# Performance work log

Measured on AMD Instinct MI355X. Metric: run time of the kernel, lower is better.

Reference implementation:

```python
import jax, jax.numpy as jnp
import numpy as np

LAYERS, BLOCKS = 10, 4
NL = LAYERS * BLOCKS
RC, DC, SC, OUT_C = 32, 32, 256, 256
B, T = 4, 32768


def setup_inputs() -> dict:
    key = jax.random.key(0)
    ks = jax.random.split(key, 6)
    s = 0.1  # keep tanh out of saturation
    return {
        "x": jax.random.normal(ks[0], (B, 1, T), jnp.float32),
        "W_start": jax.random.normal(ks[1], (RC, 1), jnp.float32) * s,
        "b_start": jnp.zeros((RC,), jnp.float32),
        "Wd": jax.random.normal(ks[2], (NL, DC, RC, 2), jnp.float32) * s,  # torch conv1d weight (out,in,k)
        "bd": jnp.zeros((NL, DC), jnp.float32),
        "Wr": jax.random.normal(ks[3], (NL, RC, DC), jnp.float32) * s,     # 1x1 residual convs
        "br": jnp.zeros((NL, RC), jnp.float32),
        "Ws": jax.random.normal(ks[4], (NL, SC, DC), jnp.float32) * s,     # 1x1 skip convs
        "bs": jnp.zeros((NL, SC), jnp.float32),
        "Wf": jax.random.normal(ks[5], (OUT_C, SC), jnp.float32) * s,      # final 1x1 conv
        "bf": jnp.zeros((OUT_C,), jnp.float32),
    }


def _forward(x, W_start, b_start, Wd, bd, Wr, br, Ws, bs, Wf, bf):
    # start 1x1 conv: [B,1,T] -> [B,RC,T]
    h = jnp.einsum('oi,bit->bot', W_start, x) + b_start[:, None]
    skip = jnp.zeros((x.shape[0], SC, x.shape[2]), x.dtype)
    for i in range(NL):  # fixed small layer loop (40)
        d = 2 ** (i % LAYERS)
        # causal dilated conv, kernel=2: out[t] = W[...,0]@x[t-d] + W[...,1]@x[t]
        h_shift = jnp.pad(h, ((0, 0), (0, 0), (d, 0)))[:, :, : h.shape[2]]
        z = (jnp.einsum('oi,bit->bot', Wd[i, :, :, 1], h)
             + jnp.einsum('oi,bit->bot', Wd[i, :, :, 0], h_shift)
             + bd[i][:, None])
        z = jnp.tanh(z)
        r = jnp.einsum('oi,bit->bot', Wr[i], z) + br[i][:, None]
        h = h + r  # residual connection
        skip = skip + jnp.einsum('oi,bit->bot', Ws[i], h) + bs[i][:, None]
    out = jax.nn.relu(skip)
    return jnp.einsum('oi,bit->bot', Wf, out) + bf[:, None]


def reference(x, W_start, b_start, Wd, bd, Wr, br, Ws, bs, Wf, bf):
    return _forward(x, W_start, b_start, Wd, bd, Wr, br, Ws, bs, Wf, bf)
```

## Files before the change

### kernel.cpp

```cpp
#include <hip/hip_runtime.h>
#include <hip/hip_bf16.h>

#define T_LEN 32768
#define B_N   4
#define RC    32
#define DC    32
#define SC    256
#define OUTC  256
#define NL    40
#define KTOT  (NL * RC)
#define NBT   (B_N * T_LEN)
#define SLOTB ((size_t)NBT * 32 * 2)
#define BTW   128
#define RING  24576

typedef float f32x4 __attribute__((ext_vector_type(4)));
typedef short bf16x8 __attribute__((ext_vector_type(8)));
typedef __attribute__((address_space(3))) unsigned int lds_u32;
typedef __attribute__((address_space(3))) char lds_char;
typedef __attribute__((address_space(1))) unsigned int glb_u32;

__device__ __forceinline__ unsigned short f2bf_bits(float f) {
    __hip_bfloat16 b = __float2bfloat16(f);
    unsigned short u;
    __builtin_memcpy(&u, &b, 2);
    return u;
}
__device__ __forceinline__ unsigned pack2(float a, float b) {
    return (unsigned)f2bf_bits(a) | ((unsigned)f2bf_bits(b) << 16);
}
__device__ __forceinline__ float bflo(unsigned u) { return __uint_as_float((u & 0xFFFFu) << 16); }
__device__ __forceinline__ float bfhi(unsigned u) { return __uint_as_float(u & 0xFFFF0000u); }
__device__ __forceinline__ float ftanh(float x) {
    float e = __expf(2.f * x);
    return 1.f - 2.f / (e + 1.f);
}
__device__ __forceinline__ int swz(int L) { return L ^ ((((L >> 7) & 3)) << 4); }

__global__ __launch_bounds__(256) void k_prep(const float* __restrict__ Ws,
                                              const float* __restrict__ Wf,
                                              const float* __restrict__ Wd,
                                              const float* __restrict__ Wr,
                                              const float* __restrict__ bs,
                                              unsigned short* __restrict__ Wsk2,
                                              unsigned short* __restrict__ Wfk,
                                              unsigned short* __restrict__ Wd1k,
                                              unsigned short* __restrict__ Wd0k,
                                              unsigned short* __restrict__ Wrk,
                                              float* __restrict__ bs_sum) {
    int g = blockIdx.x * 256 + threadIdx.x;
    if (g < SC * KTOT) {
        int i = g >> 13, r = g & 8191;
        int oc = r >> 5, c = r & 31;
        Wsk2[g] = f2bf_bits(Ws[(i * SC + oc) * RC + c]);
        return;
    }
    g -= SC * KTOT;
    if (g < OUTC * SC) { Wfk[g] = f2bf_bits(Wf[g]); return; }
    g -= OUTC * SC;
    if (g < NL * 1024) {
        int i = g >> 10, r = g & 1023;
        int o = r >> 5, c = r & 31;
        Wd1k[g] = f2bf_bits(Wd[((i * DC + o) * RC + c) * 2 + 1]);
        return;
    }
    g -= NL * 1024;
    if (g < NL * 1024) {
        int i = g >> 10, r = g & 1023;
        int o = r >> 5, c = r & 31;
        Wd0k[g] = f2bf_bits(Wd[((i * DC + o) * RC + c) * 2 + 0]);
        return;
    }
    g -= NL * 1024;
    if (g < NL * 1024) { Wrk[g] = f2bf_bits(Wr[g]); return; }
    g -= NL * 1024;
    if (g < SC) {
        float s = 0.f;
        for (int i = 0; i < NL; ++i) s += bs[i * SC + g];
        bs_sum[g] = s;
    }
}

__global__ __launch_bounds__(256) void k_start(const float* __restrict__ x,
                                               const float* __restrict__ Wst,
                                               const float* __restrict__ bst,
                                               unsigned short* __restrict__ h0) {
    int g = blockIdx.x * 256 + threadIdx.x;
    float xv = x[g];
    unsigned u[16];
#pragma unroll
    for (int q = 0; q < 16; ++q) {
        float a = Wst[2 * q] * xv + bst[2 * q];
        float b = Wst[2 * q + 1] * xv + bst[2 * q + 1];
        u[q] = pack2(a, b);
    }
    unsigned short* op = h0 + (size_t)g * 32;
#pragma unroll
    for (int q = 0; q < 4; ++q) *(uint4*)&op[q * 8] = *(uint4*)&u[q * 4];
}

__global__ __launch_bounds__(256, 4) void k_layer(const unsigned short* __restrict__ hprev,
                                                  unsigned short* __restrict__ hnext,
                                                  const unsigned short* __restrict__ Wd1k,
                                                  const unsigned short* __restrict__ Wd0k,
                                                  const unsigned short* __restrict__ Wrk,
                                                  const float* __restrict__ bd,
                                                  const float* __restrict__ br,
                                                  int d) {
    __shared__ unsigned short zbuf[4][32 * 40];
    int lane = threadIdx.x & 63;
    int wq = threadIdx.x >> 6;
    int lr = lane & 15, lg = lane >> 4;
    int btb = blockIdx.x * 128 + wq * 32;
    unsigned short* zp = &zbuf[wq][0];

    bf16x8 wd1[2], wd0[2], wr[2];
#pragma unroll
    for (int m = 0; m < 2; ++m) {
        int ao = (m * 16 + lr) * 32 + 8 * lg;
        wd1[m] = *(const bf16x8*)(Wd1k + ao);
        wd0[m] = *(const bf16x8*)(Wd0k + ao);
        wr[m]  = *(const bf16x8*)(Wrk + ao);
    }

    bf16x8 hc[2], hs[2];
    uint2 hcc[2][2];
#pragma unroll
    for (int n = 0; n < 2; ++n) {
        int bt = btb + n * 16 + lr;
        int t = bt & (T_LEN - 1);
        const unsigned short* hp = hprev + (size_t)bt * 32;
        hc[n] = *(const bf16x8*)(hp + 8 * lg);
        int bts = (t >= d) ? (bt - d) : bt;
        bf16x8 v = *(const bf16x8*)(hprev + (size_t)bts * 32 + 8 * lg);
        if (t < d) v = (bf16x8){0, 0, 0, 0, 0, 0, 0, 0};
        hs[n] = v;
#pragma unroll
        for (int m = 0; m < 2; ++m) hcc[n][m] = *(const uint2*)(hp + m * 16 + 4 * lg);
    }

    f32x4 zac[2][2];
#pragma unroll
    for (int m = 0; m < 2; ++m)
#pragma unroll
        for (int n = 0; n < 2; ++n) {
            f32x4 a = __builtin_amdgcn_mfma_f32_16x16x32_bf16(wd0[m], hs[n], (f32x4){0.f, 0.f, 0.f, 0.f}, 0, 0, 0);
            zac[m][n] = __builtin_amdgcn_mfma_f32_16x16x32_bf16(wd1[m], hc[n], a, 0, 0, 0);
        }

#pragma unroll
    for (int m = 0; m < 2; ++m) {
        float4 bdv = *(const float4*)(bd + m * 16 + 4 * lg);
#pragma unroll
        for (int n = 0; n < 2; ++n) {
            int rbt = n * 16 + lr;
            float z0 = ftanh(zac[m][n][0] + bdv.x);
            float z1 = ftanh(zac[m][n][1] + bdv.y);
            float z2 = ftanh(zac[m][n][2] + bdv.z);
            float z3 = ftanh(zac[m][n][3] + bdv.w);
            uint2 u;
            u.x = pack2(z0, z1);
            u.y = pack2(z2, z3);
            *(uint2*)(zp + rbt * 40 + m * 16 + 4 * lg) = u;
        }
    }

    f32x4 racc[2][2];
#pragma unroll
    for (int n = 0; n < 2; ++n) {
        int rbt = n * 16 + lr;
        bf16x8 zb = *(const bf16x8*)(zp + rbt * 40 + 8 * lg);
#pragma unroll
        for (int m = 0; m < 2; ++m)
            racc[m][n] = __builtin_amdgcn_mfma_f32_16x16x32_bf16(wr[m], zb, (f32x4){0.f, 0.f, 0.f, 0.f}, 0, 0, 0);
    }

#pragma unroll
    for (int m = 0; m < 2; ++m) {
        float4 brv = *(const float4*)(br + m * 16 + 4 * lg);
#pragma unroll
        for (int n = 0; n < 2; ++n) {
            int bt = btb + n * 16 + lr;
            float h0 = bflo(hcc[n][m].x) + racc[m][n][0] + brv.x;
            float h1 = bfhi(hcc[n][m].x) + racc[m][n][1] + brv.y;
            float h2 = bflo(hcc[n][m].y) + racc[m][n][2] + brv.z;
            float h3 = bfhi(hcc[n][m].y) + racc[m][n][3] + brv.w;
            uint2 u;
            u.x = pack2(h0, h1);
            u.y = pack2(h2, h3);
            *(uint2*)(hnext + (size_t)bt * 32 + m * 16 + 4 * lg) = u;
        }
    }
}

__global__ __launch_bounds__(512, 4) void k_skipfinal(const unsigned short* __restrict__ hist,
                                                      const unsigned short* __restrict__ Wsk2,
                                                      const unsigned short* __restrict__ Wfk,
                                                      const float* __restrict__ bs_sum,
                                                      const float* __restrict__ bfv,
                                                      float* __restrict__ outp) {
    __shared__ char smem[65536];
    const int tid = threadIdx.x;
    const int lane = tid & 63, wq = tid >> 6;
    const int lr = lane & 15, lg = lane >> 4;
    const int wm = wq & 3, wn = wq >> 2;
    const int bt0 = blockIdx.x * BTW;
    const char* histb = (const char*)hist;
    const char* Wsb = (const char*)Wsk2;
    lds_char* smem3 = (lds_char*)smem;

    int asrc[2], bsrc;
#pragma unroll
    for (int p = 0; p < 2; ++p) asrc[p] = swz(p * 8192 + tid * 16);
    bsrc = (size_t)0;
    {
        int D = tid * 16;
        bsrc = bt0 * 64 + swz(D);
    }

    auto stage = [&](int k) {
        char* base = smem + (k & 1) * RING;
#pragma unroll
        for (int p = 0; p < 2; ++p)
            __builtin_amdgcn_global_load_lds((const glb_u32*)(Wsb + (size_t)k * 16384 + asrc[p]),
                                             (lds_u32*)(base + p * 8192 + tid * 16), 16, 0, 0);
        __builtin_amdgcn_global_load_lds((const glb_u32*)(histb + (size_t)k * SLOTB + bsrc),
                                         (lds_u32*)(base + 16384 + tid * 16), 16, 0, 0);
    };

    f32x4 acc[4][4];
#pragma unroll
    for (int m = 0; m < 4; ++m)
#pragma unroll
        for (int n = 0; n < 4; ++n) acc[m][n] = (f32x4){0.f, 0.f, 0.f, 0.f};

    const int cswz = (lg * 16) ^ (((lr >> 1) & 3) << 4);
    const int arow = wm * 64 + lr;
    const int brow = wn * 64 + lr;

    stage(0);
    stage(1);

#pragma unroll
    for (int i = 0; i < NL; ++i) {
        if (i >= 1 && i + 1 < NL) stage(i + 1);
        if (i + 1 < NL) asm volatile("s_waitcnt vmcnt(3)" ::: "memory");
        else            asm volatile("s_waitcnt vmcnt(0)" ::: "memory");
        __builtin_amdgcn_s_barrier();

        lds_char* Ab = smem3 + (i & 1) * RING;
        lds_char* Bb = Ab + 16384;
        bf16x8 af0, af1, af2, af3, bb0, bb1, bb2, bb3;
        asm volatile("ds_read_b128 %0, %1" : "=v"(af0) : "v"(Ab + (arow + 0) * 64 + cswz));
        asm volatile("ds_read_b128 %0, %1" : "=v"(af1) : "v"(Ab + (arow + 16) * 64 + cswz));
        asm volatile("ds_read_b128 %0, %1" : "=v"(af2) : "v"(Ab + (arow + 32) * 64 + cswz));
        asm volatile("ds_read_b128 %0, %1" : "=v"(af3) : "v"(Ab + (arow + 48) * 64 + cswz));
        asm volatile("ds_read_b128 %0, %1" : "=v"(bb0) : "v"(Bb + (brow + 0) * 64 + cswz));
        asm volatile("ds_read_b128 %0, %1" : "=v"(bb1) : "v"(Bb + (brow + 16) * 64 + cswz));
        asm volatile("ds_read_b128 %0, %1" : "=v"(bb2) : "v"(Bb + (brow + 32) * 64 + cswz));
        asm volatile("ds_read_b128 %0, %1" : "=v"(bb3) : "v"(Bb + (brow + 48) * 64 + cswz));
        asm volatile("s_waitcnt lgkmcnt(0)" ::: "memory");
        __builtin_amdgcn_sched_barrier(0);

        acc[0][0] = __builtin_amdgcn_mfma_f32_16x16x32_bf16(af0, bb0, acc[0][0], 0, 0, 0);
        acc[1][0] = __builtin_amdgcn_mfma_f32_16x16x32_bf16(af1, bb0, acc[1][0], 0, 0, 0);
        acc[2][0] = __builtin_amdgcn_mfma_f32_16x16x32_bf16(af2, bb0, acc[2][0], 0, 0, 0);
        acc[3][0] = __builtin_amdgcn_mfma_f32_16x16x32_bf16(af3, bb0, acc[3][0], 0, 0, 0);
        acc[0][1] = __builtin_amdgcn_mfma_f32_16x16x32_bf16(af0, bb1, acc[0][1], 0, 0, 0);
        acc[1][1] = __builtin_amdgcn_mfma_f32_16x16x32_bf16(af1, bb1, acc[1][1], 0, 0, 0);
        acc[2][1] = __builtin_amdgcn_mfma_f32_16x16x32_bf16(af2, bb1, acc[2][1], 0, 0, 0);
        acc[3][1] = __builtin_amdgcn_mfma_f32_16x16x32_bf16(af3, bb1, acc[3][1], 0, 0, 0);
        acc[0][2] = __builtin_amdgcn_mfma_f32_16x16x32_bf16(af0, bb2, acc[0][2], 0, 0, 0);
        acc[1][2] = __builtin_amdgcn_mfma_f32_16x16x32_bf16(af1, bb2, acc[1][2], 0, 0, 0);
        acc[2][2] = __builtin_amdgcn_mfma_f32_16x16x32_bf16(af2, bb2, acc[2][2], 0, 0, 0);
        acc[3][2] = __builtin_amdgcn_mfma_f32_16x16x32_bf16(af3, bb2, acc[3][2], 0, 0, 0);
        acc[0][3] = __builtin_amdgcn_mfma_f32_16x16x32_bf16(af0, bb3, acc[0][3], 0, 0, 0);
        acc[1][3] = __builtin_amdgcn_mfma_f32_16x16x32_bf16(af1, bb3, acc[1][3], 0, 0, 0);
        acc[2][3] = __builtin_amdgcn_mfma_f32_16x16x32_bf16(af2, bb3, acc[2][3], 0, 0, 0);
        acc[3][3] = __builtin_amdgcn_mfma_f32_16x16x32_bf16(af3, bb3, acc[3][3], 0, 0, 0);
        __builtin_amdgcn_s_barrier();
    }
    __syncthreads();

    char* skb = smem;
#pragma unroll
    for (int m = 0; m < 4; ++m) {
        int oc0 = wm * 64 + m * 16 + lg * 4;
        float c0 = bs_sum[oc0], c1 = bs_sum[oc0 + 1], c2 = bs_sum[oc0 + 2], c3 = bs_sum[oc0 + 3];
#pragma unroll
        for (int n = 0; n < 4; ++n) {
            int bt = wn * 64 + n * 16 + lr;
            f32x4 v = acc[m][n];
            uint2 u;
            u.x = pack2(fmaxf(v[0] + c0, 0.f), fmaxf(v[1] + c1, 0.f));
            u.y = pack2(fmaxf(v[2] + c2, 0.f), fmaxf(v[3] + c3, 0.f));
            int L = bt * 512 + oc0 * 2;
            *(uint2*)(skb + (L ^ ((bt & 7) << 4))) = u;
        }
    }
    __syncthreads();

    f32x4 acc2[4][4];
#pragma unroll
    for (int m = 0; m < 4; ++m)
#pragma unroll
        for (int n = 0; n < 4; ++n) acc2[m][n] = (f32x4){0.f, 0.f, 0.f, 0.f};

    const unsigned short* Fb = Wfk + (size_t)(wm * 64 + lr) * SC + 8 * lg;

#pragma unroll
    for (int kk = 0; kk < SC / 32; ++kk) {
        bf16x8 fa[4];
#pragma unroll
        for (int m = 0; m < 4; ++m) fa[m] = *(const bf16x8*)(Fb + (size_t)m * 16 * SC + kk * 32);
        bf16x8 sbv[4];
#pragma unroll
        for (int n = 0; n < 4; ++n) {
            int bt = wn * 64 + n * 16 + lr;
            int L = bt * 512 + kk * 64 + lg * 16;
            sbv[n] = *(const bf16x8*)(skb + (L ^ ((bt & 7) << 4)));
        }
#pragma unroll
        for (int m = 0; m < 4; ++m)
#pragma unroll
            for (int n = 0; n < 4; ++n)
                acc2[m][n] = __builtin_amdgcn_mfma_f32_16x16x32_bf16(fa[m], sbv[n], acc2[m][n], 0, 0, 0);
    }

    int b2 = bt0 >> 15;
    int t0 = bt0 & (T_LEN - 1);
#pragma unroll
    for (int m = 0; m < 4; ++m) {
        int o0 = wm * 64 + m * 16 + lg * 4;
        float q0 = bfv[o0], q1 = bfv[o0 + 1], q2 = bfv[o0 + 2], q3 = bfv[o0 + 3];
#pragma unroll
        for (int n = 0; n < 4; ++n) {
            int t = t0 + wn * 64 + n * 16 + lr;
            f32x4 v = acc2[m][n];
            outp[((size_t)(b2 * OUTC + o0 + 0) << 15) + t] = v[0] + q0;
            outp[((size_t)(b2 * OUTC + o0 + 1) << 15) + t] = v[1] + q1;
            outp[((size_t)(b2 * OUTC + o0 + 2) << 15) + t] = v[2] + q2;
            outp[((size_t)(b2 * OUTC + o0 + 3) << 15) + t] = v[3] + q3;
        }
    }
}

extern "C" void kernel_launch(void* const* d_in, const int* in_sizes, int n_in,
                              void* d_out, int out_size, void* d_ws, size_t ws_size,
                              hipStream_t stream) {
    const float* x       = (const float*)d_in[0];
    const float* W_start = (const float*)d_in[1];
    const float* b_start = (const float*)d_in[2];
    const float* Wd      = (const float*)d_in[3];
    const float* bd      = (const float*)d_in[4];
    const float* Wr      = (const float*)d_in[5];
    const float* br      = (const float*)d_in[6];
    const float* Ws      = (const float*)d_in[7];
    const float* bs      = (const float*)d_in[8];
    const float* Wf      = (const float*)d_in[9];
    const float* bfv     = (const float*)d_in[10];

    char* wsb = (char*)d_ws;
    unsigned short* Wsk2 = (unsigned short*)(wsb);
    unsigned short* Wfk  = (unsigned short*)(wsb + 655360);
    unsigned short* Wd1k = (unsigned short*)(wsb + 786432);
    unsigned short* Wd0k = (unsigned short*)(wsb + 868352);
    unsigned short* Wrk  = (unsigned short*)(wsb + 950272);
    float*          bs_sum = (float*)(wsb + 1032192);
    char* S1 = wsb + (1 << 20);
    char* X  = S1 + 40 * SLOTB;

    auto slotptr = [&](int i) -> unsigned short* {
        return (unsigned short*)(i == 0 ? X : S1 + (size_t)(i - 1) * SLOTB);
    };

    k_prep<<<(SC * KTOT + OUTC * SC + 3 * NL * 1024 + SC + 255) / 256, 256, 0, stream>>>(
        Ws, Wf, Wd, Wr, bs, Wsk2, Wfk, Wd1k, Wd0k, Wrk, bs_sum);
    k_start<<<NBT / 256, 256, 0, stream>>>(x, W_start, b_start, slotptr(0));

    for (int i = 0; i < NL; ++i) {
        int d = 1 << (i % 10);
        k_layer<<<NBT / 128, 256, 0, stream>>>(slotptr(i), slotptr(i + 1),
                                               Wd1k + i * 1024, Wd0k + i * 1024, Wrk + i * 1024,
                                               bd + i * DC, br + i * RC, d);
    }

    k_skipfinal<<<NBT / BTW, 512, 0, stream>>>((unsigned short*)S1, Wsk2, Wfk, bs_sum, bfv, (float*)d_out);
}
```

Before: 448.4 us.

## Deepen skip-GEMM prefetch pipeline and double per-wave tile in layer kernel

The skip/final kernel now keeps separate LDS rings for weight tiles (2 stages) and history tiles (4 stages). It issues the loads for later stages after the LDS reads of the current stage, so global loads overlap the MFMA work, with vmcnt waits tuned per iteration. The layer kernel processes 64 timesteps per wave instead of 32, which halves the grid and amortizes weight loads, at the cost of more registers (launch bounds lowered to 3 blocks per SIMD). The hand-counted vmcnt schedule is fragile and could race if the load counts are wrong.

```diff
diff --git a/kernel.cpp b/kernel.cpp
--- a/kernel.cpp
+++ b/kernel.cpp
@@ -12,7 +12,6 @@
 #define NBT   (B_N * T_LEN)
 #define SLOTB ((size_t)NBT * 32 * 2)
 #define BTW   128
-#define RING  24576
 
 typedef float f32x4 __attribute__((ext_vector_type(4)));
 typedef short bf16x8 __attribute__((ext_vector_type(8)));
@@ -36,6 +35,16 @@
     return 1.f - 2.f / (e + 1.f);
 }
 __device__ __forceinline__ int swz(int L) { return L ^ ((((L >> 7) & 3)) << 4); }
+__device__ __forceinline__ void wait_vmcnt(int n) {
+    switch (n) {
+        case 0: asm volatile("s_waitcnt vmcnt(0)" ::: "memory"); break;
+        case 2: asm volatile("s_waitcnt vmcnt(2)" ::: "memory"); break;
+        case 3: asm volatile("s_waitcnt vmcnt(3)" ::: "memory"); break;
+        case 4: asm volatile("s_waitcnt vmcnt(4)" ::: "memory"); break;
+        case 5: asm volatile("s_waitcnt vmcnt(5)" ::: "memory"); break;
+        default: asm volatile("s_waitcnt vmcnt(8)" ::: "memory"); break;
+    }
+}
 
 __global__ __launch_bounds__(256) void k_prep(const float* __restrict__ Ws,
                                               const float* __restrict__ Wf,
@@ -99,7 +108,7 @@
     for (int q = 0; q < 4; ++q) *(uint4*)&op[q * 8] = *(uint4*)&u[q * 4];
 }
 
-__global__ __launch_bounds__(256, 4) void k_layer(const unsigned short* __restrict__ hprev,
+__global__ __launch_bounds__(256, 3) void k_layer(const unsigned short* __restrict__ hprev,
                                                   unsigned short* __restrict__ hnext,
                                                   const unsigned short* __restrict__ Wd1k,
                                                   const unsigned short* __restrict__ Wd0k,
@@ -107,11 +116,11 @@
                                                   const float* __restrict__ bd,
                                                   const float* __restrict__ br,
                                                   int d) {
-    __shared__ unsigned short zbuf[4][32 * 40];
+    __shared__ unsigned short zbuf[4][64 * 40];
     int lane = threadIdx.x & 63;
     int wq = threadIdx.x >> 6;
     int lr = lane & 15, lg = lane >> 4;
-    int btb = blockIdx.x * 128 + wq * 32;
+    int btb = blockIdx.x * 256 + wq * 64;
     unsigned short* zp = &zbuf[wq][0];
 
     bf16x8 wd1[2], wd0[2], wr[2];
@@ -123,10 +132,10 @@
         wr[m]  = *(const bf16x8*)(Wrk + ao);
     }
 
-    bf16x8 hc[2], hs[2];
-    uint2 hcc[2][2];
-#pragma unroll
-    for (int n = 0; n < 2; ++n) {
+    bf16x8 hc[4], hs[4];
+    uint2 hcc[4][2];
+#pragma unroll
+    for (int n = 0; n < 4; ++n) {
         int bt = btb + n * 16 + lr;
         int t = bt & (T_LEN - 1);
         const unsigned short* hp = hprev + (size_t)bt * 32;
@@ -139,11 +148,11 @@
         for (int m = 0; m < 2; ++m) hcc[n][m] = *(const uint2*)(hp + m * 16 + 4 * lg);
     }
 
-    f32x4 zac[2][2];
+    f32x4 zac[2][4];
 #pragma unroll
     for (int m = 0; m < 2; ++m)
 #pragma unroll
-        for (int n = 0; n < 2; ++n) {
+        for (int n = 0; n < 4; ++n) {
             f32x4 a = __builtin_amdgcn_mfma_f32_16x16x32_bf16(wd0[m], hs[n], (f32x4){0.f, 0.f, 0.f, 0.f}, 0, 0, 0);
             zac[m][n] = __builtin_amdgcn_mfma_f32_16x16x32_bf16(wd1[m], hc[n], a, 0, 0, 0);
         }
@@ -152,7 +161,7 @@
     for (int m = 0; m < 2; ++m) {
         float4 bdv = *(const float4*)(bd + m * 16 + 4 * lg);
 #pragma unroll
-        for (int n = 0; n < 2; ++n) {
+        for (int n = 0; n < 4; ++n) {
             int rbt = n * 16 + lr;
             float z0 = ftanh(zac[m][n][0] + bdv.x);
             float z1 = ftanh(zac[m][n][1] + bdv.y);
@@ -165,9 +174,9 @@
         }
     }
 
-    f32x4 racc[2][2];
-#pragma unroll
-    for (int n = 0; n < 2; ++n) {
+    f32x4 racc[2][4];
+#pragma unroll
+    for (int n = 0; n < 4; ++n) {
         int rbt = n * 16 + lr;
         bf16x8 zb = *(const bf16x8*)(zp + rbt * 40 + 8 * lg);
 #pragma unroll
@@ -179,7 +188,7 @@
     for (int m = 0; m < 2; ++m) {
         float4 brv = *(const float4*)(br + m * 16 + 4 * lg);
 #pragma unroll
-        for (int n = 0; n < 2; ++n) {
+        for (int n = 0; n < 4; ++n) {
             int bt = btb + n * 16 + lr;
             float h0 = bflo(hcc[n][m].x) + racc[m][n][0] + brv.x;
             float h1 = bfhi(hcc[n][m].x) + racc[m][n][1] + brv.y;
@@ -209,23 +218,22 @@
     const char* Wsb = (const char*)Wsk2;
     lds_char* smem3 = (lds_char*)smem;
 
-    int asrc[2], bsrc;
+    int asrc[2];
 #pragma unroll
     for (int p = 0; p < 2; ++p) asrc[p] = swz(p * 8192 + tid * 16);
-    bsrc = (size_t)0;
-    {
-        int D = tid * 16;
-        bsrc = bt0 * 64 + swz(D);
-    }
-
-    auto stage = [&](int k) {
-        char* base = smem + (k & 1) * RING;
+    const int bsrc = bt0 * 64 + swz(tid * 16);
+
+    auto stageA = [&](int k) {
+        char* base = smem + (k & 1) * 16384;
 #pragma unroll
         for (int p = 0; p < 2; ++p)
             __builtin_amdgcn_global_load_lds((const glb_u32*)(Wsb + (size_t)k * 16384 + asrc[p]),
                                              (lds_u32*)(base + p * 8192 + tid * 16), 16, 0, 0);
+    };
+    auto stageB = [&](int k) {
+        char* base = smem + 32768 + (k & 3) * 8192;
         __builtin_amdgcn_global_load_lds((const glb_u32*)(histb + (size_t)k * SLOTB + bsrc),
-                                         (lds_u32*)(base + 16384 + tid * 16), 16, 0, 0);
+                                         (lds_u32*)(base + tid * 16), 16, 0, 0);
     };
 
     f32x4 acc[4][4];
@@ -238,18 +246,15 @@
     const int arow = wm * 64 + lr;
     const int brow = wn * 64 + lr;
 
-    stage(0);
-    stage(1);
+    stageA(0); stageA(1);
+    stageB(0); stageB(1); stageB(2); stageB(3);
+    wait_vmcnt(3);
+    __builtin_amdgcn_s_barrier();
 
 #pragma unroll
     for (int i = 0; i < NL; ++i) {
-        if (i >= 1 && i + 1 < NL) stage(i + 1);
-        if (i + 1 < NL) asm volatile("s_waitcnt vmcnt(3)" ::: "memory");
-        else            asm volatile("s_waitcnt vmcnt(0)" ::: "memory");
-        __builtin_amdgcn_s_barrier();
-
-        lds_char* Ab = smem3 + (i & 1) * RING;
-        lds_char* Bb = Ab + 16384;
+        lds_char* Ab = smem3 + (i & 1) * 16384;
+        lds_char* Bb = smem3 + 32768 + (i & 3) * 8192;
         bf16x8 af0, af1, af2, af3, bb0, bb1, bb2, bb3;
         asm volatile("ds_read_b128 %0, %1" : "=v"(af0) : "v"(Ab + (arow + 0) * 64 + cswz));
         asm volatile("ds_read_b128 %0, %1" : "=v"(af1) : "v"(Ab + (arow + 16) * 64 + cswz));
@@ -261,6 +266,10 @@
         asm volatile("ds_read_b128 %0, %1" : "=v"(bb3) : "v"(Bb + (brow + 48) * 64 + cswz));
         asm volatile("s_waitcnt lgkmcnt(0)" ::: "memory");
         __builtin_amdgcn_sched_barrier(0);
+        __builtin_amdgcn_s_barrier();
+
+        if (i + 2 < NL) stageA(i + 2);
+        if (i + 4 < NL) stageB(i + 4);
 
         acc[0][0] = __builtin_amdgcn_mfma_f32_16x16x32_bf16(af0, bb0, acc[0][0], 0, 0, 0);
         acc[1][0] = __builtin_amdgcn_mfma_f32_16x16x32_bf16(af1, bb0, acc[1][0], 0, 0, 0);
@@ -278,7 +287,12 @@
         acc[1][3] = __builtin_amdgcn_mfma_f32_16x16x32_bf16(af1, bb3, acc[1][3], 0, 0, 0);
         acc[2][3] = __builtin_amdgcn_mfma_f32_16x16x32_bf16(af2, bb3, acc[2][3], 0, 0, 0);
         acc[3][3] = __builtin_amdgcn_mfma_f32_16x16x32_bf16(af3, bb3, acc[3][3], 0, 0, 0);
-        __builtin_amdgcn_s_barrier();
+
+        if (i < NL - 1) {
+            int Nw = (i == 0) ? 5 : (i <= 35) ? 4 : (i == 36) ? 3 : (i == 37) ? 2 : 0;
+            wait_vmcnt(Nw);
+            __builtin_amdgcn_s_barrier();
+        }
     }
     __syncthreads();
 
@@ -380,7 +394,7 @@
 
     for (int i = 0; i < NL; ++i) {
         int d = 1 << (i % 10);
-        k_layer<<<NBT / 128, 256, 0, stream>>>(slotptr(i), slotptr(i + 1),
+        k_layer<<<NBT / 256, 256, 0, stream>>>(slotptr(i), slotptr(i + 1),
                                                Wd1k + i * 1024, Wd0k + i * 1024, Wrk + i * 1024,
                                                bd + i * DC, br + i * RC, d);
     }
```

Result: slower. 503.0 us (+12.2%).

## Fuse all forty residual layers into one persistent kernel with neighbor flags

Applied to the files above, without the earlier changes.

The forty per-layer launches are replaced by a single persistent kernel with one 512-thread block per (512-timestep chunk, batch). Each block runs every layer on its chunk in order. A release/acquire flag chain makes a block wait until the previous chunk has finished the prior layer, which is enough because the dilation never exceeds the chunk length. This is meant to remove per-layer launch and tail overhead and to keep each chunk's activations hot in cache between layers. In exchange the grid is much smaller, blocks are serialized along a dependency chain that adds pipeline skew, and the kernel relies on all blocks being co-resident to avoid deadlock.

```diff
diff --git a/kernel.cpp b/kernel.cpp
--- a/kernel.cpp
+++ b/kernel.cpp
@@ -99,97 +99,112 @@
     for (int q = 0; q < 4; ++q) *(uint4*)&op[q * 8] = *(uint4*)&u[q * 4];
 }
 
-__global__ __launch_bounds__(256, 4) void k_layer(const unsigned short* __restrict__ hprev,
-                                                  unsigned short* __restrict__ hnext,
-                                                  const unsigned short* __restrict__ Wd1k,
-                                                  const unsigned short* __restrict__ Wd0k,
-                                                  const unsigned short* __restrict__ Wrk,
-                                                  const float* __restrict__ bd,
-                                                  const float* __restrict__ br,
-                                                  int d) {
-    __shared__ unsigned short zbuf[4][32 * 40];
-    int lane = threadIdx.x & 63;
-    int wq = threadIdx.x >> 6;
-    int lr = lane & 15, lg = lane >> 4;
-    int btb = blockIdx.x * 128 + wq * 32;
-    unsigned short* zp = &zbuf[wq][0];
-
+__global__ __launch_bounds__(512) void k_zeroflags(int* __restrict__ flags) {
+    flags[blockIdx.x * 512 + threadIdx.x] = 0;
+}
+
+__device__ __forceinline__ void layer_step(const unsigned short* __restrict__ slotin,
+                                           unsigned short* __restrict__ slotout,
+                                           const unsigned short* __restrict__ w1p,
+                                           const unsigned short* __restrict__ w0p,
+                                           const unsigned short* __restrict__ wrp,
+                                           const float* __restrict__ bdp,
+                                           const float* __restrict__ brp,
+                                           unsigned short* zp, int tbase, int b,
+                                           int lr, int lg, int d) {
     bf16x8 wd1[2], wd0[2], wr[2];
+    float4 bdv[2], brv[2];
 #pragma unroll
     for (int m = 0; m < 2; ++m) {
         int ao = (m * 16 + lr) * 32 + 8 * lg;
-        wd1[m] = *(const bf16x8*)(Wd1k + ao);
-        wd0[m] = *(const bf16x8*)(Wd0k + ao);
-        wr[m]  = *(const bf16x8*)(Wrk + ao);
-    }
-
-    bf16x8 hc[2], hs[2];
-    uint2 hcc[2][2];
-#pragma unroll
-    for (int n = 0; n < 2; ++n) {
-        int bt = btb + n * 16 + lr;
-        int t = bt & (T_LEN - 1);
-        const unsigned short* hp = hprev + (size_t)bt * 32;
-        hc[n] = *(const bf16x8*)(hp + 8 * lg);
-        int bts = (t >= d) ? (bt - d) : bt;
-        bf16x8 v = *(const bf16x8*)(hprev + (size_t)bts * 32 + 8 * lg);
-        if (t < d) v = (bf16x8){0, 0, 0, 0, 0, 0, 0, 0};
-        hs[n] = v;
-#pragma unroll
-        for (int m = 0; m < 2; ++m) hcc[n][m] = *(const uint2*)(hp + m * 16 + 4 * lg);
-    }
-
-    f32x4 zac[2][2];
-#pragma unroll
-    for (int m = 0; m < 2; ++m)
-#pragma unroll
-        for (int n = 0; n < 2; ++n) {
-            f32x4 a = __builtin_amdgcn_mfma_f32_16x16x32_bf16(wd0[m], hs[n], (f32x4){0.f, 0.f, 0.f, 0.f}, 0, 0, 0);
-            zac[m][n] = __builtin_amdgcn_mfma_f32_16x16x32_bf16(wd1[m], hc[n], a, 0, 0, 0);
-        }
-
-#pragma unroll
-    for (int m = 0; m < 2; ++m) {
-        float4 bdv = *(const float4*)(bd + m * 16 + 4 * lg);
-#pragma unroll
-        for (int n = 0; n < 2; ++n) {
-            int rbt = n * 16 + lr;
-            float z0 = ftanh(zac[m][n][0] + bdv.x);
-            float z1 = ftanh(zac[m][n][1] + bdv.y);
-            float z2 = ftanh(zac[m][n][2] + bdv.z);
-            float z3 = ftanh(zac[m][n][3] + bdv.w);
-            uint2 u;
-            u.x = pack2(z0, z1);
-            u.y = pack2(z2, z3);
-            *(uint2*)(zp + rbt * 40 + m * 16 + 4 * lg) = u;
-        }
-    }
-
-    f32x4 racc[2][2];
-#pragma unroll
-    for (int n = 0; n < 2; ++n) {
-        int rbt = n * 16 + lr;
-        bf16x8 zb = *(const bf16x8*)(zp + rbt * 40 + 8 * lg);
-#pragma unroll
-        for (int m = 0; m < 2; ++m)
-            racc[m][n] = __builtin_amdgcn_mfma_f32_16x16x32_bf16(wr[m], zb, (f32x4){0.f, 0.f, 0.f, 0.f}, 0, 0, 0);
-    }
-
-#pragma unroll
-    for (int m = 0; m < 2; ++m) {
-        float4 brv = *(const float4*)(br + m * 16 + 4 * lg);
-#pragma unroll
-        for (int n = 0; n < 2; ++n) {
-            int bt = btb + n * 16 + lr;
-            float h0 = bflo(hcc[n][m].x) + racc[m][n][0] + brv.x;
-            float h1 = bfhi(hcc[n][m].x) + racc[m][n][1] + brv.y;
-            float h2 = bflo(hcc[n][m].y) + racc[m][n][2] + brv.z;
-            float h3 = bfhi(hcc[n][m].y) + racc[m][n][3] + brv.w;
-            uint2 u;
-            u.x = pack2(h0, h1);
-            u.y = pack2(h2, h3);
-            *(uint2*)(hnext + (size_t)bt * 32 + m * 16 + 4 * lg) = u;
-        }
+        wd1[m] = *(const bf16x8*)(w1p + ao);
+        wd0[m] = *(const bf16x8*)(w0p + ao);
+        wr[m]  = *(const bf16x8*)(wrp + ao);
+        bdv[m] = *(const float4*)(bdp + m * 16 + 4 * lg);
+        brv[m] = *(const float4*)(brp + m * 16 + 4 * lg);
+    }
+#pragma unroll
+    for (int n = 0; n < 4; ++n) {
+        int t = tbase + n * 16 + lr;
+        size_t bt = ((size_t)b << 15) + t;
+        const unsigned short* hp = slotin + bt * 32;
+        bf16x8 hc = *(const bf16x8*)(hp + 8 * lg);
+        uint2 hcc0 = *(const uint2*)(hp + 4 * lg);
+        uint2 hcc1 = *(const uint2*)(hp + 16 + 4 * lg);
+        bf16x8 hs = (bf16x8){0, 0, 0, 0, 0, 0, 0, 0};
+        if (t >= d) hs = *(const bf16x8*)(hp - (size_t)d * 32 + 8 * lg);
+
+        f32x4 z0 = __builtin_amdgcn_mfma_f32_16x16x32_bf16(wd0[0], hs, (f32x4){0.f, 0.f, 0.f, 0.f}, 0, 0, 0);
+        z0 = __builtin_amdgcn_mfma_f32_16x16x32_bf16(wd1[0], hc, z0, 0, 0, 0);
+        f32x4 z1 = __builtin_amdgcn_mfma_f32_16x16x32_bf16(wd0[1], hs, (f32x4){0.f, 0.f, 0.f, 0.f}, 0, 0, 0);
+        z1 = __builtin_amdgcn_mfma_f32_16x16x32_bf16(wd1[1], hc, z1, 0, 0, 0);
+
+        uint2 u0, u1;
+        u0.x = pack2(ftanh(z0[0] + bdv[0].x), ftanh(z0[1] + bdv[0].y));
+        u0.y = pack2(ftanh(z0[2] + bdv[0].z), ftanh(z0[3] + bdv[0].w));
+        u1.x = pack2(ftanh(z1[0] + bdv[1].x), ftanh(z1[1] + bdv[1].y));
+        u1.y = pack2(ftanh(z1[2] + bdv[1].z), ftanh(z1[3] + bdv[1].w));
+        *(uint2*)(zp + lr * 40 + 4 * lg) = u0;
+        *(uint2*)(zp + lr * 40 + 16 + 4 * lg) = u1;
+
+        bf16x8 zb = *(const bf16x8*)(zp + lr * 40 + 8 * lg);
+        f32x4 r0 = __builtin_amdgcn_mfma_f32_16x16x32_bf16(wr[0], zb, (f32x4){0.f, 0.f, 0.f, 0.f}, 0, 0, 0);
+        f32x4 r1 = __builtin_amdgcn_mfma_f32_16x16x32_bf16(wr[1], zb, (f32x4){0.f, 0.f, 0.f, 0.f}, 0, 0, 0);
+
+        uint2 o0, o1;
+        o0.x = pack2(bflo(hcc0.x) + r0[0] + brv[0].x, bfhi(hcc0.x) + r0[1] + brv[0].y);
+        o0.y = pack2(bflo(hcc0.y) + r0[2] + brv[0].z, bfhi(hcc0.y) + r0[3] + brv[0].w);
+        o1.x = pack2(bflo(hcc1.x) + r1[0] + brv[1].x, bfhi(hcc1.x) + r1[1] + brv[1].y);
+        o1.y = pack2(bflo(hcc1.y) + r1[2] + brv[1].z, bfhi(hcc1.y) + r1[3] + brv[1].w);
+        unsigned short* op = slotout + bt * 32;
+        *(uint2*)(op + 4 * lg) = o0;
+        *(uint2*)(op + 16 + 4 * lg) = o1;
+    }
+}
+
+__global__ __launch_bounds__(512, 2) void k_pipe(const unsigned short* __restrict__ slot0,
+                                                 unsigned short* __restrict__ S1h,
+                                                 const unsigned short* __restrict__ Wd1k,
+                                                 const unsigned short* __restrict__ Wd0k,
+                                                 const unsigned short* __restrict__ Wrk,
+                                                 const float* __restrict__ bd,
+                                                 const float* __restrict__ br,
+                                                 int* __restrict__ flags) {
+    __shared__ unsigned short zbuf[8][16 * 40];
+    const int tid = threadIdx.x;
+    const int lane = tid & 63, wq = tid >> 6;
+    const int lr = lane & 15, lg = lane >> 4;
+    const int c = blockIdx.x, b = blockIdx.y;
+    const int blk = b * 64 + c;
+    unsigned short* zp = &zbuf[wq][0];
+    const int tbase = c * 512 + wq * 64;
+    const size_t SLOTE = SLOTB / 2;
+
+    layer_step(slot0, S1h, Wd1k, Wd0k, Wrk, bd, br, zp, tbase, b, lr, lg, 1);
+    __syncthreads();
+    if (tid == 0) {
+        __hip_atomic_store(flags + blk * 8, 1, __ATOMIC_RELEASE, __HIP_MEMORY_SCOPE_AGENT);
+        if (c > 0) {
+            while (__hip_atomic_load(flags + (blk - 1) * 8, __ATOMIC_ACQUIRE, __HIP_MEMORY_SCOPE_AGENT) < 1)
+                __builtin_amdgcn_s_sleep(2);
+        }
+    }
+    __syncthreads();
+
+    for (int i = 1; i < NL; ++i) {
+        int d = 1 << (i % 10);
+        layer_step(S1h + (size_t)(i - 1) * SLOTE, S1h + (size_t)i * SLOTE,
+                   Wd1k + i * 1024, Wd0k + i * 1024, Wrk + i * 1024,
+                   bd + i * DC, br + i * RC, zp, tbase, b, lr, lg, d);
+        __syncthreads();
+        if (tid == 0 && i < NL - 1) {
+            __hip_atomic_store(flags + blk * 8, i + 1, __ATOMIC_RELEASE, __HIP_MEMORY_SCOPE_AGENT);
+            if (c > 0) {
+                while (__hip_atomic_load(flags + (blk - 1) * 8, __ATOMIC_ACQUIRE, __HIP_MEMORY_SCOPE_AGENT) < i + 1)
+                    __builtin_amdgcn_s_sleep(2);
+            }
+        }
+        __syncthreads();
     }
 }
 
@@ -212,7 +227,6 @@
     int asrc[2], bsrc;
 #pragma unroll
     for (int p = 0; p < 2; ++p) asrc[p] = swz(p * 8192 + tid * 16);
-    bsrc = (size_t)0;
     {
         int D = tid * 16;
         bsrc = bt0 * 64 + swz(D);
@@ -367,23 +381,18 @@
     unsigned short* Wd0k = (unsigned short*)(wsb + 868352);
     unsigned short* Wrk  = (unsigned short*)(wsb + 950272);
     float*          bs_sum = (float*)(wsb + 1032192);
+    int*            flags  = (int*)(wsb + 1033216);
     char* S1 = wsb + (1 << 20);
     char* X  = S1 + 40 * SLOTB;
 
-    auto slotptr = [&](int i) -> unsigned short* {
-        return (unsigned short*)(i == 0 ? X : S1 + (size_t)(i - 1) * SLOTB);
-    };
-
     k_prep<<<(SC * KTOT + OUTC * SC + 3 * NL * 1024 + SC + 255) / 256, 256, 0, stream>>>(
         Ws, Wf, Wd, Wr, bs, Wsk2, Wfk, Wd1k, Wd0k, Wrk, bs_sum);
-    k_start<<<NBT / 256, 256, 0, stream>>>(x, W_start, b_start, slotptr(0));
-
-    for (int i = 0; i < NL; ++i) {
-        int d = 1 << (i % 10);
-        k_layer<<<NBT / 128, 256, 0, stream>>>(slotptr(i), slotptr(i + 1),
-                                               Wd1k + i * 1024, Wd0k + i * 1024, Wrk + i * 1024,
-                                               bd + i * DC, br + i * RC, d);
-    }
+    k_start<<<NBT / 256, 256, 0, stream>>>(x, W_start, b_start, (unsigned short*)X);
+    k_zeroflags<<<4, 512, 0, stream>>>(flags);
+
+    dim3 gp(T_LEN / 512, B_N);
+    k_pipe<<<gp, 512, 0, stream>>>((const unsigned short*)X, (unsigned short*)S1,
+                                   Wd1k, Wd0k, Wrk, bd, br, flags);
 
     k_skipfinal<<<NBT / BTW, 512, 0, stream>>>((unsigned short*)S1, Wsk2, Wfk, bs_sum, bfv, (float*)d_out);
 }
```

Result: slower. 975.0 us (+117.4%).

## Fuse each dilation block of ten layers into one LDS-resident kernel with halo

Applied to the files above, without the earlier changes.

Replaces forty per-layer launches with four launches, one per block of ten dilations. Each workgroup loads a 512-step tile plus a 1024-step causal halo into LDS and runs all ten layers in place, shrinking the computed window as the dilation grows. Per-layer hidden states are still written out for the skip kernel. This removes the global reload of h before every layer and most launch overhead, at the cost of recomputing the halo region and using 1024-thread workgroups with large LDS.

```diff
diff --git a/kernel.cpp b/kernel.cpp
--- a/kernel.cpp
+++ b/kernel.cpp
@@ -11,8 +11,10 @@
 #define KTOT  (NL * RC)
 #define NBT   (B_N * T_LEN)
 #define SLOTB ((size_t)NBT * 32 * 2)
+#define SLOTE ((size_t)NBT * 32)
 #define BTW   128
 #define RING  24576
+#define GT    1536
 
 typedef float f32x4 __attribute__((ext_vector_type(4)));
 typedef short bf16x8 __attribute__((ext_vector_type(8)));
@@ -36,6 +38,9 @@
     return 1.f - 2.f / (e + 1.f);
 }
 __device__ __forceinline__ int swz(int L) { return L ^ ((((L >> 7) & 3)) << 4); }
+__device__ __forceinline__ int lcol(int u, int colbyte) {
+    return colbyte ^ (((u ^ (u >> 2)) & 3) << 4);
+}
 
 __global__ __launch_bounds__(256) void k_prep(const float* __restrict__ Ws,
                                               const float* __restrict__ Wf,
@@ -99,98 +104,139 @@
     for (int q = 0; q < 4; ++q) *(uint4*)&op[q * 8] = *(uint4*)&u[q * 4];
 }
 
-__global__ __launch_bounds__(256, 4) void k_layer(const unsigned short* __restrict__ hprev,
-                                                  unsigned short* __restrict__ hnext,
-                                                  const unsigned short* __restrict__ Wd1k,
-                                                  const unsigned short* __restrict__ Wd0k,
-                                                  const unsigned short* __restrict__ Wrk,
-                                                  const float* __restrict__ bd,
-                                                  const float* __restrict__ br,
-                                                  int d) {
-    __shared__ unsigned short zbuf[4][32 * 40];
-    int lane = threadIdx.x & 63;
-    int wq = threadIdx.x >> 6;
-    int lr = lane & 15, lg = lane >> 4;
-    int btb = blockIdx.x * 128 + wq * 32;
-    unsigned short* zp = &zbuf[wq][0];
-
+template<int NT>
+__device__ __forceinline__ void group_layer(unsigned short* hbuf,
+                                            unsigned short* zp,
+                                            const unsigned short* __restrict__ w1g,
+                                            const unsigned short* __restrict__ w0g,
+                                            const unsigned short* __restrict__ wrg,
+                                            const float* __restrict__ bdp,
+                                            const float* __restrict__ brp,
+                                            unsigned short* __restrict__ slotj,
+                                            int t0, int b, int wq, int lr, int lg, int d) {
     bf16x8 wd1[2], wd0[2], wr[2];
+    float4 bdv[2], brv[2];
 #pragma unroll
     for (int m = 0; m < 2; ++m) {
         int ao = (m * 16 + lr) * 32 + 8 * lg;
-        wd1[m] = *(const bf16x8*)(Wd1k + ao);
-        wd0[m] = *(const bf16x8*)(Wd0k + ao);
-        wr[m]  = *(const bf16x8*)(Wrk + ao);
-    }
-
-    bf16x8 hc[2], hs[2];
-    uint2 hcc[2][2];
-#pragma unroll
-    for (int n = 0; n < 2; ++n) {
-        int bt = btb + n * 16 + lr;
-        int t = bt & (T_LEN - 1);
-        const unsigned short* hp = hprev + (size_t)bt * 32;
-        hc[n] = *(const bf16x8*)(hp + 8 * lg);
-        int bts = (t >= d) ? (bt - d) : bt;
-        bf16x8 v = *(const bf16x8*)(hprev + (size_t)bts * 32 + 8 * lg);
-        if (t < d) v = (bf16x8){0, 0, 0, 0, 0, 0, 0, 0};
-        hs[n] = v;
-#pragma unroll
-        for (int m = 0; m < 2; ++m) hcc[n][m] = *(const uint2*)(hp + m * 16 + 4 * lg);
-    }
-
-    f32x4 zac[2][2];
-#pragma unroll
-    for (int m = 0; m < 2; ++m)
+        wd1[m] = *(const bf16x8*)(w1g + ao);
+        wd0[m] = *(const bf16x8*)(w0g + ao);
+        wr[m]  = *(const bf16x8*)(wrg + ao);
+        bdv[m] = *(const float4*)(bdp + m * 16 + 4 * lg);
+        brv[m] = *(const float4*)(brp + m * 16 + 4 * lg);
+    }
+    const int u0 = GT - (NT << 9);
+
+    bf16x8 hs[NT][2];
+#pragma unroll
+    for (int p = 0; p < NT; ++p) {
+        int ut = u0 + (wq + (p << 4)) * 32;
 #pragma unroll
         for (int n = 0; n < 2; ++n) {
-            f32x4 a = __builtin_amdgcn_mfma_f32_16x16x32_bf16(wd0[m], hs[n], (f32x4){0.f, 0.f, 0.f, 0.f}, 0, 0, 0);
-            zac[m][n] = __builtin_amdgcn_mfma_f32_16x16x32_bf16(wd1[m], hc[n], a, 0, 0, 0);
-        }
-
-#pragma unroll
-    for (int m = 0; m < 2; ++m) {
-        float4 bdv = *(const float4*)(bd + m * 16 + 4 * lg);
+            int u = ut + n * 16 + lr;
+            int t = t0 + u - 1024;
+            int us = u - d; if (us < 0) us = 0;
+            bf16x8 v = *(const bf16x8*)((const char*)hbuf + us * 64 + lcol(us, lg * 16));
+            if (t < d) v = (bf16x8){0, 0, 0, 0, 0, 0, 0, 0};
+            hs[p][n] = v;
+        }
+    }
+    __syncthreads();
+
+#pragma unroll
+    for (int p = 0; p < NT; ++p) {
+        const int ut = u0 + (wq + (p << 4)) * 32;
+        bf16x8 hcv[2];
+        uint2 hccv[2][2];
 #pragma unroll
         for (int n = 0; n < 2; ++n) {
-            int rbt = n * 16 + lr;
-            float z0 = ftanh(zac[m][n][0] + bdv.x);
-            float z1 = ftanh(zac[m][n][1] + bdv.y);
-            float z2 = ftanh(zac[m][n][2] + bdv.z);
-            float z3 = ftanh(zac[m][n][3] + bdv.w);
-            uint2 u;
-            u.x = pack2(z0, z1);
-            u.y = pack2(z2, z3);
-            *(uint2*)(zp + rbt * 40 + m * 16 + 4 * lg) = u;
-        }
-    }
-
-    f32x4 racc[2][2];
-#pragma unroll
-    for (int n = 0; n < 2; ++n) {
-        int rbt = n * 16 + lr;
-        bf16x8 zb = *(const bf16x8*)(zp + rbt * 40 + 8 * lg);
+            int u = ut + n * 16 + lr;
+            hcv[n] = *(const bf16x8*)((const char*)hbuf + u * 64 + lcol(u, lg * 16));
+#pragma unroll
+            for (int m = 0; m < 2; ++m)
+                hccv[n][m] = *(const uint2*)((const char*)hbuf + u * 64 + lcol(u, m * 32 + lg * 8));
+        }
+        f32x4 zac[2][2];
 #pragma unroll
         for (int m = 0; m < 2; ++m)
-            racc[m][n] = __builtin_amdgcn_mfma_f32_16x16x32_bf16(wr[m], zb, (f32x4){0.f, 0.f, 0.f, 0.f}, 0, 0, 0);
-    }
-
-#pragma unroll
-    for (int m = 0; m < 2; ++m) {
-        float4 brv = *(const float4*)(br + m * 16 + 4 * lg);
+#pragma unroll
+            for (int n = 0; n < 2; ++n) {
+                f32x4 a = __builtin_amdgcn_mfma_f32_16x16x32_bf16(wd0[m], hs[p][n], (f32x4){0.f, 0.f, 0.f, 0.f}, 0, 0, 0);
+                zac[m][n] = __builtin_amdgcn_mfma_f32_16x16x32_bf16(wd1[m], hcv[n], a, 0, 0, 0);
+            }
+#pragma unroll
+        for (int m = 0; m < 2; ++m)
+#pragma unroll
+            for (int n = 0; n < 2; ++n) {
+                int rbt = n * 16 + lr;
+                uint2 uu;
+                uu.x = pack2(ftanh(zac[m][n][0] + bdv[m].x), ftanh(zac[m][n][1] + bdv[m].y));
+                uu.y = pack2(ftanh(zac[m][n][2] + bdv[m].z), ftanh(zac[m][n][3] + bdv[m].w));
+                *(uint2*)(zp + rbt * 40 + m * 16 + 4 * lg) = uu;
+            }
+        f32x4 racc[2][2];
 #pragma unroll
         for (int n = 0; n < 2; ++n) {
-            int bt = btb + n * 16 + lr;
-            float h0 = bflo(hcc[n][m].x) + racc[m][n][0] + brv.x;
-            float h1 = bfhi(hcc[n][m].x) + racc[m][n][1] + brv.y;
-            float h2 = bflo(hcc[n][m].y) + racc[m][n][2] + brv.z;
-            float h3 = bfhi(hcc[n][m].y) + racc[m][n][3] + brv.w;
-            uint2 u;
-            u.x = pack2(h0, h1);
-            u.y = pack2(h2, h3);
-            *(uint2*)(hnext + (size_t)bt * 32 + m * 16 + 4 * lg) = u;
-        }
-    }
+            bf16x8 zb = *(const bf16x8*)(zp + (n * 16 + lr) * 40 + 8 * lg);
+#pragma unroll
+            for (int m = 0; m < 2; ++m)
+                racc[m][n] = __builtin_amdgcn_mfma_f32_16x16x32_bf16(wr[m], zb, (f32x4){0.f, 0.f, 0.f, 0.f}, 0, 0, 0);
+        }
+#pragma unroll
+        for (int m = 0; m < 2; ++m)
+#pragma unroll
+            for (int n = 0; n < 2; ++n) {
+                int u = ut + n * 16 + lr;
+                uint2 o;
+                o.x = pack2(bflo(hccv[n][m].x) + racc[m][n][0] + brv[m].x,
+                            bfhi(hccv[n][m].x) + racc[m][n][1] + brv[m].y);
+                o.y = pack2(bflo(hccv[n][m].y) + racc[m][n][2] + brv[m].z,
+                            bfhi(hccv[n][m].y) + racc[m][n][3] + brv[m].w);
+                *(uint2*)((char*)hbuf + u * 64 + lcol(u, m * 32 + lg * 8)) = o;
+                if (p == NT - 1) {
+                    int t = t0 + u - 1024;
+                    *(uint2*)(slotj + ((size_t)b * T_LEN + t) * 32 + m * 16 + 4 * lg) = o;
+                }
+            }
+    }
+    __syncthreads();
+}
+
+__global__ __launch_bounds__(1024) void k_group(const unsigned short* __restrict__ slot_prev,
+                                                unsigned short* __restrict__ slot_base,
+                                                const unsigned short* __restrict__ Wd1g,
+                                                const unsigned short* __restrict__ Wd0g,
+                                                const unsigned short* __restrict__ Wrg,
+                                                const float* __restrict__ bdg,
+                                                const float* __restrict__ brg) {
+    __shared__ unsigned short hbuf[GT * 32];
+    __shared__ unsigned short zbuf[16][32 * 40];
+    const int tid = threadIdx.x;
+    const int lane = tid & 63, wq = tid >> 6;
+    const int lr = lane & 15, lg = lane >> 4;
+    const int t0 = blockIdx.x * 512, b = blockIdx.y;
+    unsigned short* zp = &zbuf[wq][0];
+
+    for (int f = tid; f < GT * 4; f += 1024) {
+        int u = f >> 2, part = f & 3;
+        int t = t0 + u - 1024;
+        uint4 v = {0u, 0u, 0u, 0u};
+        if (t >= 0) v = *(const uint4*)(slot_prev + ((size_t)b * T_LEN + t) * 32 + part * 8);
+        *(uint4*)((char*)hbuf + u * 64 + lcol(u, part * 16)) = v;
+    }
+    __syncthreads();
+
+#pragma unroll 1
+    for (int j = 0; j < 8; ++j)
+        group_layer<3>(hbuf, zp, Wd1g + j * 1024, Wd0g + j * 1024, Wrg + j * 1024,
+                       bdg + j * 32, brg + j * 32,
+                       slot_base + (size_t)j * SLOTE, t0, b, wq, lr, lg, 1 << j);
+    group_layer<2>(hbuf, zp, Wd1g + 8 * 1024, Wd0g + 8 * 1024, Wrg + 8 * 1024,
+                   bdg + 8 * 32, brg + 8 * 32,
+                   slot_base + (size_t)8 * SLOTE, t0, b, wq, lr, lg, 256);
+    group_layer<1>(hbuf, zp, Wd1g + 9 * 1024, Wd0g + 9 * 1024, Wrg + 9 * 1024,
+                   bdg + 9 * 32, brg + 9 * 32,
+                   slot_base + (size_t)9 * SLOTE, t0, b, wq, lr, lg, 512);
 }
 
 __global__ __launch_bounds__(512, 4) void k_skipfinal(const unsigned short* __restrict__ hist,
@@ -212,7 +258,6 @@
     int asrc[2], bsrc;
 #pragma unroll
     for (int p = 0; p < 2; ++p) asrc[p] = swz(p * 8192 + tid * 16);
-    bsrc = (size_t)0;
     {
         int D = tid * 16;
         bsrc = bt0 * 64 + swz(D);
@@ -370,19 +415,18 @@
     char* S1 = wsb + (1 << 20);
     char* X  = S1 + 40 * SLOTB;
 
-    auto slotptr = [&](int i) -> unsigned short* {
-        return (unsigned short*)(i == 0 ? X : S1 + (size_t)(i - 1) * SLOTB);
-    };
-
     k_prep<<<(SC * KTOT + OUTC * SC + 3 * NL * 1024 + SC + 255) / 256, 256, 0, stream>>>(
         Ws, Wf, Wd, Wr, bs, Wsk2, Wfk, Wd1k, Wd0k, Wrk, bs_sum);
-    k_start<<<NBT / 256, 256, 0, stream>>>(x, W_start, b_start, slotptr(0));
-
-    for (int i = 0; i < NL; ++i) {
-        int d = 1 << (i % 10);
-        k_layer<<<NBT / 128, 256, 0, stream>>>(slotptr(i), slotptr(i + 1),
-                                               Wd1k + i * 1024, Wd0k + i * 1024, Wrk + i * 1024,
-                                               bd + i * DC, br + i * RC, d);
+    k_start<<<NBT / 256, 256, 0, stream>>>(x, W_start, b_start, (unsigned short*)X);
+
+    for (int g = 0; g < 4; ++g) {
+        const unsigned short* prev = (g == 0)
+            ? (const unsigned short*)X
+            : (const unsigned short*)(S1 + (size_t)(10 * g - 1) * SLOTB);
+        k_group<<<dim3(T_LEN / 512, B_N), 1024, 0, stream>>>(
+            prev, (unsigned short*)(S1 + (size_t)(10 * g) * SLOTB),
+            Wd1k + g * 10 * 1024, Wd0k + g * 10 * 1024, Wrk + g * 10 * 1024,
+            bd + g * 10 * 32, br + g * 10 * 32);
     }
 
     k_skipfinal<<<NBT / BTW, 512, 0, stream>>>((unsigned short*)S1, Wsk2, Wfk, bs_sum, bfv, (float*)d_out);
```

New measurement: 755.9 us. 68.6% more time.
